# Optimization experiments

Measured on AMD Instinct MI355X. Metric: run time of the kernel, lower is better.

## Reference

```python
import jax, jax.numpy as jnp
import numpy as np

N_A, N_B, D = 200_000, 400_000, 128
E1, E2 = 800_000, 800_000
UPDATE_KEEP = 0.5   # update_keep_prob
FEAT_KEEP = 0.3     # feature_keep_prob
LN_EPS = 1e-5


def setup_inputs() -> dict:
    key = jax.random.key(0)
    ks = jax.random.split(key, 22)
    s = 0.05  # weight scale
    f32 = jnp.float32
    return {
        "feats_A": jax.random.normal(ks[0], (N_A, D), f32),
        "feats_B": jax.random.normal(ks[1], (N_B, D), f32),
        "W_p2c": jax.random.normal(ks[2], (D, D), f32) * s,
        "b_p2c": jnp.zeros((D,), f32),
        "W_c2p": jax.random.normal(ks[3], (D, D), f32) * s,
        "b_c2p": jnp.zeros((D,), f32),
        "Wself_A": jax.random.normal(ks[4], (D, D), f32) * s,
        "bself_A": jnp.zeros((D,), f32),
        "lnw_A": jnp.ones((D,), f32),
        "lnb_A": jnp.zeros((D,), f32),
        "Wself_B": jax.random.normal(ks[5], (D, D), f32) * s,
        "bself_B": jnp.zeros((D,), f32),
        "lnw_B": jnp.ones((D,), f32),
        "lnb_B": jnp.zeros((D,), f32),
        "u_p2c": jax.random.uniform(ks[6], (E1, 1), f32),
        "u_c2p": jax.random.uniform(ks[7], (E2, 1), f32),
        "u_feat_A": jax.random.uniform(ks[8], (D,), f32),
        "u_feat_B": jax.random.uniform(ks[9], (D,), f32),
        "src_p2c": jax.random.randint(ks[10], (E1,), 0, N_A, jnp.int32),
        "dst_p2c": jax.random.randint(ks[11], (E1,), 0, N_B, jnp.int32),
        "src_c2p": jax.random.randint(ks[12], (E2,), 0, N_B, jnp.int32),
        "dst_c2p": jax.random.randint(ks[13], (E2,), 0, N_A, jnp.int32),
    }


def _edge_aggregate(src_feat, src_idx, dst_idx, W, b, u_edge, n_dst):
    # gather -> per-edge-type linear -> bernoulli update mask -> scatter-add
    msg = src_feat[src_idx] @ W.T + b                     # [E, D]
    um = (u_edge < UPDATE_KEEP).astype(src_feat.dtype)    # [E, 1]
    msg = msg * um
    agg = jax.ops.segment_sum(msg, dst_idx, num_segments=n_dst)       # [n_dst, D]
    deg = jax.ops.segment_sum(um[:, 0], dst_idx, num_segments=n_dst)  # [n_dst]
    return agg, deg


def _table_update(feats, agg, deg, Wself, bself, lnw, lnb, u_feat):
    deg = jnp.maximum(deg, 1.0)[:, None]
    fmask = (u_feat < FEAT_KEEP).astype(feats.dtype)      # [D], bernoulli(0.3)
    agg = (agg / deg) * fmask
    comb = feats @ Wself.T + bself + agg
    mu = jnp.mean(comb, axis=-1, keepdims=True)
    var = jnp.var(comb, axis=-1, keepdims=True)
    comb = (comb - mu) * jax.lax.rsqrt(var + LN_EPS) * lnw + lnb
    comb = jax.nn.selu(comb + feats)                      # residual (Identity proj) + SELU
    # write back only masked feature columns
    return jnp.where(fmask > 0.5, comb, feats)


def reference(feats_A, feats_B, W_p2c, b_p2c, W_c2p, b_c2p,
              Wself_A, bself_A, lnw_A, lnb_A,
              Wself_B, bself_B, lnw_B, lnb_B,
              u_p2c, u_c2p, u_feat_A, u_feat_B,
              src_p2c, dst_p2c, src_c2p, dst_c2p):
    # PARENT_TO_CHILD: A -> B ; CHILD_TO_PARENT: B -> A
    agg_B, deg_B = _edge_aggregate(feats_A, src_p2c, dst_p2c, W_p2c, b_p2c, u_p2c, N_B)
    agg_A, deg_A = _edge_aggregate(feats_B, src_c2p, dst_c2p, W_c2p, b_c2p, u_c2p, N_A)
    out_A = _table_update(feats_A, agg_A, deg_A, Wself_A, bself_A, lnw_A, lnb_A, u_feat_A)
    out_B = _table_update(feats_B, agg_B, deg_B, Wself_B, bself_B, lnw_B, lnb_B, u_feat_B)
    return (out_A, out_B)
```

## Files before the change

### kernel.cpp

```cpp
#include <hip/hip_runtime.h>
#include <hip/hip_bf16.h>

#define DD 128

typedef __attribute__((ext_vector_type(8))) short short8;
typedef __attribute__((ext_vector_type(8))) unsigned short u16x8;
typedef __attribute__((ext_vector_type(4))) unsigned short u16x4;
typedef __attribute__((ext_vector_type(4))) float f32x4;

__device__ __forceinline__ unsigned short f2bf(float f) {
    union { unsigned int u; float f; } c; c.f = f;
    unsigned int u = c.u;
    unsigned int r = (u + 0x7FFFu + ((u >> 16) & 1u)) >> 16;
    return (unsigned short)r;
}
__device__ __forceinline__ float bf2f(unsigned short h) {
    union { unsigned int u; float f; } c; c.u = ((unsigned int)h) << 16; return c.f;
}

__device__ __forceinline__ void scatter_dir(const float* __restrict__ feats,
                                            const int* __restrict__ src,
                                            const int* __restrict__ dst,
                                            const float* __restrict__ u,
                                            unsigned int* __restrict__ pre,
                                            float* __restrict__ deg,
                                            int E, int wave, int lane, int nw)
{
    for (int e = wave; e < E; e += nw) {
        if (u[e] < 0.5f) {
            int s = src[e], d = dst[e];
            float2 x = *(const float2*)(feats + (size_t)s * DD + 2 * lane);
            unsigned int* p = pre + (size_t)d * 64 + lane;
#if defined(__HIP_DEVICE_COMPILE__)
            typedef short sv2 __attribute__((ext_vector_type(2)));
            sv2 v; v[0] = (short)f2bf(x.x); v[1] = (short)f2bf(x.y);
            __builtin_amdgcn_global_atomic_fadd_v2bf16((__attribute__((address_space(1))) sv2*)p, v);
#else
            (void)p; (void)x;
#endif
            if (lane == 0) unsafeAtomicAdd(deg + d, 1.0f);
        }
    }
}

__global__ void scatter2_kernel(const float* __restrict__ f1,
                                const int* __restrict__ s1, const int* __restrict__ d1,
                                const float* __restrict__ u1,
                                unsigned int* __restrict__ p1, float* __restrict__ g1, int E1,
                                const float* __restrict__ f2,
                                const int* __restrict__ s2, const int* __restrict__ d2,
                                const float* __restrict__ u2,
                                unsigned int* __restrict__ p2, float* __restrict__ g2, int E2)
{
    int half = gridDim.x >> 1;
    int lane = threadIdx.x & 63;
    int wavein = (blockIdx.x % half) * (blockDim.x >> 6) + (threadIdx.x >> 6);
    int nw = half * (blockDim.x >> 6);
    if (blockIdx.x < half) scatter_dir(f1, s1, d1, u1, p1, g1, E1, wavein, lane, nw);
    else                   scatter_dir(f2, s2, d2, u2, p2, g2, E2, wavein, lane, nw);
}

__global__ __launch_bounds__(512, 2)
void table_kernel(const float* __restrict__ feats,
                  const unsigned short* __restrict__ pre,
                  const float* __restrict__ deg,
                  const float* __restrict__ Wself,
                  const float* __restrict__ bself,
                  const float* __restrict__ Wedge,
                  const float* __restrict__ bedge,
                  const float* __restrict__ lnw,
                  const float* __restrict__ lnb,
                  const float* __restrict__ ufeat,
                  float* __restrict__ out,
                  int N)
{
    __shared__ __align__(16) unsigned short wlds[2 * 16384];
    __shared__ __align__(16) char xsall[8 * 8192];

    const int tid = threadIdx.x;

    {
        int j  = tid >> 2;
        int kq = tid & 3;
        float fm = ufeat[j] < 0.3f ? 1.0f : 0.0f;
        const float* wsrow = Wself + j * DD + kq * 32;
        const float* werow = Wedge + j * DD + kq * 32;
        char* lbs = (char*)wlds;
        #pragma unroll
        for (int c = 0; c < 4; ++c) {
            unsigned short tS[8], tE[8];
            #pragma unroll
            for (int i = 0; i < 8; ++i) {
                tS[i] = f2bf(wsrow[c * 8 + i]);
                tE[i] = f2bf(werow[c * 8 + i] * fm);
            }
            int addr = (j * 256 + kq * 64 + c * 16) ^ ((j & 7) << 4);
            *(short8*)(lbs + addr)         = *(short8*)tS;
            *(short8*)(lbs + 32768 + addr) = *(short8*)tE;
        }
    }
    __syncthreads();

    const int wave = tid >> 6;
    const int lane = tid & 63;
    const int lj = lane & 15;
    const int lk = lane >> 4;

    float bs[8], bem[8], lw[8], lb[8];
    unsigned fmask = 0;
    #pragma unroll
    for (int ct = 0; ct < 8; ++ct) {
        int col = ct * 16 + lj;
        bool fm = ufeat[col] < 0.3f;
        bs[ct]  = bself[col];
        bem[ct] = fm ? bedge[col] : 0.0f;
        lw[ct]  = lnw[col];
        lb[ct]  = lnb[col];
        fmask |= (fm ? 1u : 0u) << ct;
    }

    char* xs  = xsall + wave * 8192;
    char* ps  = xs + 4096;
    const char* wb = (const char*)wlds;
    const int ldb  = lj * 256 + lk * 16;
    const int xorv = (lj & 7) << 4;

    const int frow = lane >> 5;
    const int fc4  = lane & 31;
    const int prow = lane >> 4;
    const int pch  = lane & 15;

    const int ntiles = N >> 4;
    for (int tile = blockIdx.x * 8 + wave; tile < ntiles; tile += gridDim.x * 8) {
        int row0 = tile << 4;

        #pragma unroll
        for (int j = 0; j < 8; ++j) {
            int row = j * 2 + frow;
            f32x4 v = *(const f32x4*)(feats + (size_t)(row0 + row) * DD + fc4 * 4);
            unsigned short t4[4];
            #pragma unroll
            for (int i = 0; i < 4; ++i) t4[i] = f2bf(v[i]);
            *(u16x4*)(xs + row * 256 + ((fc4 * 8) ^ ((row & 7) << 4))) = *(u16x4*)t4;
        }
        #pragma unroll
        for (int c = 0; c < 4; ++c) {
            int row = c * 4 + prow;
            u16x8 v = *(const u16x8*)(pre + (size_t)(row0 + row) * DD + pch * 8);
            *(u16x8*)(ps + row * 256 + ((pch * 16) ^ ((row & 7) << 4))) = v;
        }

        float dgr  = deg[row0 + lj];
        float invd = 1.0f / fmaxf(dgr, 1.0f);
        float dpown = dgr > 0.5f ? 1.0f : 0.0f;

        short8 xf[4], pf[4];
        #pragma unroll
        for (int t = 0; t < 4; ++t) {
            int a = (ldb + t * 64) ^ xorv;
            xf[t] = *(const short8*)(xs + a);
            u16x8 pv = *(const u16x8*)(ps + a);
            unsigned short tp[8];
            #pragma unroll
            for (int i = 0; i < 8; ++i) tp[i] = f2bf(bf2f(pv[i]) * invd);
            pf[t] = *(short8*)tp;
        }

        f32x4 acc[8];
        #pragma unroll
        for (int ct = 0; ct < 8; ++ct) { f32x4 z = {0.f,0.f,0.f,0.f}; acc[ct] = z; }

        #pragma unroll
        for (int t = 0; t < 4; ++t) {
            int a0 = (ldb + t * 64) ^ xorv;
            #pragma unroll
            for (int ct = 0; ct < 8; ++ct) {
                short8 ws = *(const short8*)(wb + ct * 4096 + a0);
                short8 we = *(const short8*)(wb + 32768 + ct * 4096 + a0);
                acc[ct] = __builtin_amdgcn_mfma_f32_16x16x32_bf16(xf[t], ws, acc[ct], 0, 0, 0);
                acc[ct] = __builtin_amdgcn_mfma_f32_16x16x32_bf16(pf[t], we, acc[ct], 0, 0, 0);
            }
        }

        #pragma unroll
        for (int q = 0; q < 4; ++q) {
            int rrl = lk * 4 + q;
            float degpos = __shfl(dpown, rrl, 64);
            float val[8];
            float s = 0.f, s2 = 0.f;
            #pragma unroll
            for (int ct = 0; ct < 8; ++ct) {
                float v = acc[ct][q] + bs[ct] + degpos * bem[ct];
                val[ct] = v; s += v; s2 += v * v;
            }
            #pragma unroll
            for (int m = 1; m < 16; m <<= 1) {
                s  += __shfl_xor(s,  m, 64);
                s2 += __shfl_xor(s2, m, 64);
            }
            float mu   = s * (1.0f / 128.0f);
            float var  = s2 * (1.0f / 128.0f) - mu * mu;
            float rstd = rsqrtf(var + 1e-5f);
            #pragma unroll
            for (int ct = 0; ct < 8; ++ct) {
                int col = ct * 16 + lj;
                int ra  = rrl * 256 + ((col * 2) ^ ((rrl & 7) << 4));
                float fres = bf2f(*(const unsigned short*)(xs + ra));
                float ln = (val[ct] - mu) * rstd * lw[ct] + lb[ct];
                float x = ln + fres;
                float selu = x > 0.f ? 1.0507009873554805f * x
                                     : 1.0507009873554805f * 1.6732632423543772f * (expf(x) - 1.0f);
                float o = ((fmask >> ct) & 1) ? selu : fres;
                *(unsigned short*)(xs + ra) = f2bf(o);
            }
        }

        #pragma unroll
        for (int j = 0; j < 8; ++j) {
            int row = j * 2 + frow;
            u16x4 ov = *(const u16x4*)(xs + row * 256 + ((fc4 * 8) ^ ((row & 7) << 4)));
            f32x4 o;
            #pragma unroll
            for (int i = 0; i < 4; ++i) o[i] = bf2f(ov[i]);
            *(f32x4*)(out + (size_t)(row0 + row) * DD + fc4 * 4) = o;
        }
    }
}

extern "C" void kernel_launch(void* const* d_in, const int* in_sizes, int n_in,
                              void* d_out, int out_size, void* d_ws, size_t ws_size,
                              hipStream_t stream)
{
    const float* feats_A = (const float*)d_in[0];
    const float* feats_B = (const float*)d_in[1];
    const float* W_p2c   = (const float*)d_in[2];
    const float* b_p2c   = (const float*)d_in[3];
    const float* W_c2p   = (const float*)d_in[4];
    const float* b_c2p   = (const float*)d_in[5];
    const float* Wself_A = (const float*)d_in[6];
    const float* bself_A = (const float*)d_in[7];
    const float* lnw_A   = (const float*)d_in[8];
    const float* lnb_A   = (const float*)d_in[9];
    const float* Wself_B = (const float*)d_in[10];
    const float* bself_B = (const float*)d_in[11];
    const float* lnw_B   = (const float*)d_in[12];
    const float* lnb_B   = (const float*)d_in[13];
    const float* u_p2c   = (const float*)d_in[14];
    const float* u_c2p   = (const float*)d_in[15];
    const float* u_featA = (const float*)d_in[16];
    const float* u_featB = (const float*)d_in[17];
    const int* src_p2c = (const int*)d_in[18];
    const int* dst_p2c = (const int*)d_in[19];
    const int* src_c2p = (const int*)d_in[20];
    const int* dst_c2p = (const int*)d_in[21];

    const int N_A = in_sizes[0] / DD;
    const int N_B = in_sizes[1] / DD;
    const int E1  = in_sizes[14];
    const int E2  = in_sizes[15];

    float* outA = (float*)d_out;
    float* outB = outA + (size_t)N_A * DD;

    const size_t preB_bytes = (size_t)N_B * DD * 2;
    const size_t preA_bytes = (size_t)N_A * DD * 2;
    const size_t need = preB_bytes + preA_bytes + (size_t)(N_A + N_B) * 4;
    if (ws_size < need) return;

    unsigned int*   preB_w = (unsigned int*)d_ws;
    unsigned int*   preA_w = (unsigned int*)((char*)d_ws + preB_bytes);
    float*          deg_A  = (float*)((char*)d_ws + preB_bytes + preA_bytes);
    float*          deg_B  = deg_A + N_A;
    const unsigned short* preB_h = (const unsigned short*)preB_w;
    const unsigned short* preA_h = (const unsigned short*)preA_w;

    (void)hipMemsetAsync(d_ws, 0, need, stream);

    dim3 sblk(256), sgrd(2048);
    scatter2_kernel<<<sgrd, sblk, 0, stream>>>(feats_A, src_p2c, dst_p2c, u_p2c, preB_w, deg_B, E1,
                                               feats_B, src_c2p, dst_c2p, u_c2p, preA_w, deg_A, E2);

    dim3 tblk(512), tgrd(256);
    table_kernel<<<tgrd, tblk, 0, stream>>>(feats_A, preA_h, deg_A,
                                            Wself_A, bself_A, W_c2p, b_c2p,
                                            lnw_A, lnb_A, u_featA, outA, N_A);
    table_kernel<<<tgrd, tblk, 0, stream>>>(feats_B, preB_h, deg_B,
                                            Wself_B, bself_B, W_p2c, b_p2c,
                                            lnw_B, lnb_B, u_featB, outB, N_B);
}
```

Measured before the change: 859.5 us.

## Software-pipeline table kernel global loads into registers for next tile

The table kernel now prefetches the next tile's feats, precomputed aggregate and degree into registers while the current tile is being processed. This lets global-memory latency overlap with the MFMA/LayerNorm work instead of stalling at the start of each tile. The extra registers (about 48 VGPRs) force launch bounds down from 2 to 1 block per CU, so occupancy drops in exchange.

```diff
diff --git a/kernel.cpp b/kernel.cpp
--- a/kernel.cpp
+++ b/kernel.cpp
@@ -60,7 +60,7 @@
     else                   scatter_dir(f2, s2, d2, u2, p2, g2, E2, wavein, lane, nw);
 }
 
-__global__ __launch_bounds__(512, 2)
+__global__ __launch_bounds__(512, 1)
 void table_kernel(const float* __restrict__ feats,
                   const unsigned short* __restrict__ pre,
                   const float* __restrict__ deg,
@@ -131,27 +131,63 @@
     const int pch  = lane & 15;
 
     const int ntiles = N >> 4;
-    for (int tile = blockIdx.x * 8 + wave; tile < ntiles; tile += gridDim.x * 8) {
+    const int stride = gridDim.x * 8;
+    int tile = blockIdx.x * 8 + wave;
+
+    f32x4 xr[8];
+    u16x8 pw[4];
+    float dg = 0.f;
+
+    if (tile < ntiles) {
         int row0 = tile << 4;
-
         #pragma unroll
         for (int j = 0; j < 8; ++j) {
             int row = j * 2 + frow;
-            f32x4 v = *(const f32x4*)(feats + (size_t)(row0 + row) * DD + fc4 * 4);
-            unsigned short t4[4];
-            #pragma unroll
-            for (int i = 0; i < 4; ++i) t4[i] = f2bf(v[i]);
-            *(u16x4*)(xs + row * 256 + ((fc4 * 8) ^ ((row & 7) << 4))) = *(u16x4*)t4;
+            xr[j] = *(const f32x4*)(feats + (size_t)(row0 + row) * DD + fc4 * 4);
         }
         #pragma unroll
         for (int c = 0; c < 4; ++c) {
             int row = c * 4 + prow;
-            u16x8 v = *(const u16x8*)(pre + (size_t)(row0 + row) * DD + pch * 8);
-            *(u16x8*)(ps + row * 256 + ((pch * 16) ^ ((row & 7) << 4))) = v;
-        }
-
-        float dgr  = deg[row0 + lj];
-        float invd = 1.0f / fmaxf(dgr, 1.0f);
+            pw[c] = *(const u16x8*)(pre + (size_t)(row0 + row) * DD + pch * 8);
+        }
+        dg = deg[row0 + lj];
+    }
+
+    while (tile < ntiles) {
+        int row0 = tile << 4;
+        int nxt  = tile + stride;
+
+        #pragma unroll
+        for (int j = 0; j < 8; ++j) {
+            int row = j * 2 + frow;
+            unsigned short t4[4];
+            #pragma unroll
+            for (int i = 0; i < 4; ++i) t4[i] = f2bf(xr[j][i]);
+            *(u16x4*)(xs + row * 256 + ((fc4 * 8) ^ ((row & 7) << 4))) = *(u16x4*)t4;
+        }
+        #pragma unroll
+        for (int c = 0; c < 4; ++c) {
+            int row = c * 4 + prow;
+            *(u16x8*)(ps + row * 256 + ((pch * 16) ^ ((row & 7) << 4))) = pw[c];
+        }
+        float dgr = dg;
+
+        if (nxt < ntiles) {
+            int nrow0 = nxt << 4;
+            #pragma unroll
+            for (int j = 0; j < 8; ++j) {
+                int row = j * 2 + frow;
+                xr[j] = *(const f32x4*)(feats + (size_t)(nrow0 + row) * DD + fc4 * 4);
+            }
+            #pragma unroll
+            for (int c = 0; c < 4; ++c) {
+                int row = c * 4 + prow;
+                pw[c] = *(const u16x8*)(pre + (size_t)(nrow0 + row) * DD + pch * 8);
+            }
+            dg = deg[nrow0 + lj];
+        }
+
+        float invd  = 1.0f / fmaxf(dgr, 1.0f);
         float dpown = dgr > 0.5f ? 1.0f : 0.0f;
 
         short8 xf[4], pf[4];
@@ -224,6 +260,8 @@
             for (int i = 0; i < 4; ++i) o[i] = bf2f(ov[i]);
             *(f32x4*)(out + (size_t)(row0 + row) * DD + fc4 * 4) = o;
         }
+
+        tile = nxt;
     }
 }
 
```

After: 924.7 us. 7.6% more time.
